# Kernel optimization log

Measured on AMD Instinct MI355X. Metric: run time of the kernel, lower is better.

Reference implementation:

```python
import jax, jax.numpy as jnp
import numpy as np


def apply_rotary_emb(x, freqs_cis):
    # x: [B, N, H, Dh], freqs_cis: [N, Dh//2, 2]
    B, N, H, Dh = x.shape
    x2 = x.reshape(B, N, H, Dh // 2, 2)
    f = freqs_cis[None, :, None]  # [1, N, 1, Dh//2, 2]
    real = x2[..., 0] * f[..., 0] - x2[..., 1] * f[..., 1]
    imag = x2[..., 1] * f[..., 0] + x2[..., 0] * f[..., 1]
    out = jnp.stack([real, imag], axis=-1)
    return out.reshape(B, N, H, Dh).astype(x.dtype)


def setup_inputs() -> dict:
    key = jax.random.key(0)
    k1, k2, k3, k4 = jax.random.split(key, 4)
    B, N, dim, n_head = 2, 2048, 2048, 16
    head_dim = dim // n_head
    x = jax.random.normal(k1, (B, N, dim), dtype=jnp.float32)
    # realistic rotary freqs (cos/sin), though random also works for correctness
    pos = jnp.arange(N, dtype=jnp.float32)[:, None]
    inv_freq = 1.0 / (10000.0 ** (jnp.arange(0, head_dim, 2, dtype=jnp.float32) / head_dim))
    ang = pos * inv_freq[None, :]  # [N, Dh//2]
    freqs_cis = jnp.stack([jnp.cos(ang), jnp.sin(ang)], axis=-1)  # [N, Dh//2, 2]
    wqkv = jax.random.normal(k2, (dim, 3 * dim), dtype=jnp.float32) * (dim ** -0.5)
    wo = jax.random.normal(k3, (dim, dim), dtype=jnp.float32) * (dim ** -0.5)
    return {"x": x, "freqs_cis": freqs_cis, "wqkv": wqkv, "wo": wo}


def reference(x, freqs_cis, wqkv, wo):
    B, N, dim = x.shape
    n_head = 16
    head_dim = dim // n_head
    qkv = x @ wqkv  # [B, N, 3*dim]
    q, k, v = jnp.split(qkv, 3, axis=-1)
    q = q.reshape(B, N, n_head, head_dim)
    k = k.reshape(B, N, n_head, head_dim)
    v = v.reshape(B, N, n_head, head_dim)
    q = apply_rotary_emb(q, freqs_cis)
    k = apply_rotary_emb(k, freqs_cis)
    scale = 1.0 / jnp.sqrt(jnp.asarray(head_dim, dtype=q.dtype))
    scores = jnp.einsum('bqhd,bkhd->bhqk', q, k) * scale
    attn = jax.nn.softmax(scores, axis=-1)
    out = jnp.einsum('bhqk,bkhd->bqhd', attn, v).reshape(B, N, dim)
    return out @ wo
```

## Files before the change

kernel.cpp:

```cpp
#include <hip/hip_runtime.h>
#include <hip/hip_bf16.h>
#include <stdint.h>

typedef __attribute__((ext_vector_type(8))) short bf16x8;
typedef __attribute__((ext_vector_type(4))) float f32x4;
typedef __attribute__((ext_vector_type(4))) unsigned short u16x4;
typedef __attribute__((ext_vector_type(8))) unsigned short u16x8;

#define DEV __device__ __forceinline__

DEV unsigned short f2bf(float f) {
  union { __hip_bfloat16 h; unsigned short u; } cv;
  cv.h = __float2bfloat16(f);
  return cv.u;
}

DEV void gload_lds16(const void* g, void* l) {
  __builtin_amdgcn_global_load_lds(
      (__attribute__((address_space(1))) void*)(uintptr_t)g,
      (__attribute__((address_space(3))) void*)(uint32_t)(uintptr_t)l,
      16, 0, 0);
}

__global__ __launch_bounds__(256) void k_convert(const float* __restrict__ in,
                                                 unsigned short* __restrict__ out,
                                                 int n8) {
  int i = blockIdx.x * 256 + threadIdx.x;
  if (i >= n8) return;
  const float4* p = (const float4*)in + (size_t)i * 2;
  float4 a = p[0], b = p[1];
  u16x8 o;
  o[0] = f2bf(a.x); o[1] = f2bf(a.y); o[2] = f2bf(a.z); o[3] = f2bf(a.w);
  o[4] = f2bf(b.x); o[5] = f2bf(b.y); o[6] = f2bf(b.z); o[7] = f2bf(b.w);
  *((u16x8*)out + (size_t)i) = o;
}

__global__ __launch_bounds__(256) void k_transpose_bf16(const float* __restrict__ in,
                                                        unsigned short* __restrict__ out,
                                                        int R, int C) {
  __shared__ float tile[32][33];
  const int t = threadIdx.x;
  const int c0 = blockIdx.x * 32, r0 = blockIdx.y * 32;
  {
    int r = t >> 3, c4 = (t & 7) * 4;
    float4 v = *(const float4*)&in[(size_t)(r0 + r) * C + c0 + c4];
    tile[r][c4] = v.x; tile[r][c4 + 1] = v.y; tile[r][c4 + 2] = v.z; tile[r][c4 + 3] = v.w;
  }
  __syncthreads();
  int c = t >> 3, r4 = (t & 7) * 4;
  u16x4 o;
  o[0] = f2bf(tile[r4 + 0][c]); o[1] = f2bf(tile[r4 + 1][c]);
  o[2] = f2bf(tile[r4 + 2][c]); o[3] = f2bf(tile[r4 + 3][c]);
  *(u16x4*)&out[(size_t)(c0 + c) * R + r0 + r4] = o;
}

__global__ __launch_bounds__(512, 2) void k_gemm_qkv(
    const unsigned short* __restrict__ A,
    const unsigned short* __restrict__ Bt,
    unsigned short* __restrict__ qb,
    unsigned short* __restrict__ kb,
    unsigned short* __restrict__ vt,
    const float* __restrict__ freqs) {
  constexpr int Kdim = 2048;
  __shared__ unsigned short As[2][16384];
  __shared__ unsigned short Bs[2][12288];
  const int t = threadIdx.x;
  const int lane = t & 63, wid = t >> 6;
  const int l15 = lane & 15, l4 = (lane >> 4) & 3;
  const int wm = wid >> 2, wn = wid & 3;
  const int bid = blockIdx.x;
  const int wg = (bid & 7) * 64 + (bid >> 3);
  const int by = wg & 15, bx = wg >> 4;
  const int m0 = by * 256, n0 = bx * 192;

  f32x4 acc[8][3];
#pragma unroll
  for (int i = 0; i < 8; i++)
#pragma unroll
    for (int j = 0; j < 3; j++) acc[i][j] = (f32x4)0.f;

  auto stageUA = [&](unsigned short* dstUnit, const unsigned short* src, int khalf) {
#pragma unroll
    for (int cb = 0; cb < 2; cb++) {
      int slotu = cb * 512 + wid * 64;
      int slot = slotu + lane;
      int row = slot >> 2, s = slot & 3;
      int c = s ^ ((row >> 1) & 3);
      gload_lds16(src + (size_t)row * Kdim + khalf * 32 + c * 8,
                  dstUnit + slotu * 8);
    }
  };
  auto stageUB = [&](unsigned short* dstUnit, const unsigned short* src, int khalf) {
    {
      int slotu = wid * 64;
      int slot = slotu + lane;
      int row = slot >> 2, s = slot & 3;
      int c = s ^ ((row >> 1) & 3);
      gload_lds16(src + (size_t)row * Kdim + khalf * 32 + c * 8,
                  dstUnit + slotu * 8);
    }
    {
      int slotu = 512 + (wid & 3) * 64;
      int slot = slotu + lane;
      int row = slot >> 2, s = slot & 3;
      int c = s ^ ((row >> 1) & 3);
      gload_lds16(src + (size_t)row * Kdim + khalf * 32 + c * 8,
                  dstUnit + slotu * 8);
    }
  };

  auto rdA2 = [&](int buf, int kk, int mh, bf16x8 (&f)[4]) {
    const unsigned short* base = &As[buf][kk * 8192];
#pragma unroll
    for (int mi = 0; mi < 4; mi++) {
      int row = wm * 128 + mh * 64 + mi * 16 + l15;
      int s = l4 ^ ((row >> 1) & 3);
      f[mi] = *(const bf16x8*)&base[row * 32 + s * 8];
    }
  };
  auto rdB2 = [&](int buf, int kk, bf16x8 (&f)[3]) {
    const unsigned short* base = &Bs[buf][kk * 6144];
#pragma unroll
    for (int ni = 0; ni < 3; ni++) {
      int row = wn * 48 + ni * 16 + l15;
      int s = l4 ^ ((row >> 1) & 3);
      f[ni] = *(const bf16x8*)&base[row * 32 + s * 8];
    }
  };
  auto mmaP = [&](bf16x8 (&a4)[4], bf16x8 (&b3)[3], int mib) {
    __builtin_amdgcn_s_setprio(1);
#pragma unroll
    for (int mi = 0; mi < 4; mi++)
#pragma unroll
      for (int ni = 0; ni < 3; ni++)
        acc[mib + mi][ni] = __builtin_amdgcn_mfma_f32_16x16x32_bf16(
            a4[mi], b3[ni], acc[mib + mi][ni], 0, 0, 0);
    __builtin_amdgcn_s_setprio(0);
  };

  const unsigned short* Abase = A + (size_t)m0 * Kdim;
  const unsigned short* Bbase = Bt + (size_t)n0 * Kdim;

  stageUA(&As[0][0], Abase, 0);
  stageUB(&Bs[0][0], Bbase, 0);
  stageUA(&As[0][8192], Abase, 1);
  stageUB(&Bs[0][6144], Bbase, 1);
  stageUA(&As[1][0], Abase + 64, 0);
  stageUB(&Bs[1][0], Bbase + 64, 0);
  asm volatile("s_waitcnt vmcnt(8)" ::: "memory");
  __builtin_amdgcn_s_barrier();

  bf16x8 a4[4], b3[3];
  for (int j = 0; j < 32; j++) {
    const int buf = j & 1;

    rdA2(buf, 0, 0, a4);
    rdB2(buf, 0, b3);
    if (j + 1 < 32) {
      stageUA(&As[buf ^ 1][8192], Abase + (j + 1) * 64, 1);
      stageUB(&Bs[buf ^ 1][6144], Bbase + (j + 1) * 64, 1);
    }
    __builtin_amdgcn_s_barrier();
    mmaP(a4, b3, 0);
    __builtin_amdgcn_s_barrier();

    rdA2(buf, 0, 1, a4);
    __builtin_amdgcn_s_barrier();
    mmaP(a4, b3, 4);
    if (j < 31) asm volatile("s_waitcnt vmcnt(8) lgkmcnt(0)" ::: "memory");
    else        asm volatile("s_waitcnt vmcnt(0) lgkmcnt(0)" ::: "memory");
    __builtin_amdgcn_s_barrier();

    rdA2(buf, 1, 0, a4);
    rdB2(buf, 1, b3);
    if (j + 2 < 32) {
      stageUA(&As[buf][0], Abase + (j + 2) * 64, 0);
      stageUB(&Bs[buf][0], Bbase + (j + 2) * 64, 0);
    }
    __builtin_amdgcn_s_barrier();
    mmaP(a4, b3, 0);
    __builtin_amdgcn_s_barrier();

    rdA2(buf, 1, 1, a4);
    __builtin_amdgcn_s_barrier();
    mmaP(a4, b3, 4);
    if (j < 30)       asm volatile("s_waitcnt vmcnt(8) lgkmcnt(0)" ::: "memory");
    else if (j == 30) asm volatile("s_waitcnt vmcnt(4) lgkmcnt(0)" ::: "memory");
    else              asm volatile("s_waitcnt lgkmcnt(0)" ::: "memory");
    __builtin_amdgcn_s_barrier();
  }

#pragma unroll
  for (int mi = 0; mi < 8; mi++) {
    int rowb = m0 + wm * 128 + mi * 16 + l4 * 4;
    int b = rowb >> 11;
    int tok0 = rowb & 2047;
#pragma unroll
    for (int ni = 0; ni < 3; ni++) {
      int col = n0 + wn * 48 + ni * 16 + l15;
      int sec = col >> 11;
      int h = (col >> 7) & 15;
      int dh = col & 127;
      if (sec == 2) {
        u16x4 o;
#pragma unroll
        for (int r = 0; r < 4; r++) o[r] = f2bf(acc[mi][ni][r]);
        *(u16x4*)&vt[((size_t)(b * 16 + h) * 128 + dh) * 2048 + tok0] = o;
      } else {
        unsigned short* dst = (sec == 0) ? qb : kb;
        int dh2 = dh >> 1;
        int odd = dh & 1;
#pragma unroll
        for (int r = 0; r < 4; r++) {
          float v = acc[mi][ni][r];
          float p = __shfl_xor(v, 1, 64);
          float2 cs = *(const float2*)&freqs[((size_t)(tok0 + r) * 64 + dh2) * 2];
          float o = odd ? (v * cs.x + p * cs.y) : (v * cs.x - p * cs.y);
          dst[((size_t)(b * 16 + h) * 2048 + tok0 + r) * 128 + dh] = f2bf(o);
        }
      }
    }
  }
}

__global__ __launch_bounds__(256) void k_gemm_out(
    const unsigned short* __restrict__ A,
    const unsigned short* __restrict__ Bt,
    int Kdim, int Nn,
    float* __restrict__ Cout) {
  __shared__ unsigned short As[128 * 64];
  __shared__ unsigned short Bs[128 * 64];
  const int t = threadIdx.x;
  const int lane = t & 63, wid = t >> 6;
  const int l15 = lane & 15, l4 = lane >> 4;
  const int m0 = blockIdx.y * 128, n0 = blockIdx.x * 128;
  const int wr = (wid >> 1) * 64, wc = (wid & 1) * 64;

  f32x4 acc[4][4];
#pragma unroll
  for (int i = 0; i < 4; i++)
#pragma unroll
    for (int j = 0; j < 4; j++) acc[i][j] = (f32x4)0.f;

  for (int k0 = 0; k0 < Kdim; k0 += 64) {
    __syncthreads();
#pragma unroll
    for (int j = 0; j < 4; j++) {
      int slotbase = j * 256 + wid * 64;
      int slot = slotbase + lane;
      int row = slot >> 3, cc = slot & 7;
      int cg = cc ^ (row & 7);
      gload_lds16(A + (size_t)(m0 + row) * Kdim + k0 + cg * 8, &As[slotbase * 8]);
      gload_lds16(Bt + (size_t)(n0 + row) * Kdim + k0 + cg * 8, &Bs[slotbase * 8]);
    }
    __syncthreads();
#pragma unroll
    for (int kk = 0; kk < 2; kk++) {
      bf16x8 af[4], bfr[4];
#pragma unroll
      for (int mi = 0; mi < 4; mi++) {
        int row = wr + mi * 16 + l15;
        int c = (kk * 4 + l4) ^ (row & 7);
        af[mi] = *(const bf16x8*)&As[row * 64 + c * 8];
      }
#pragma unroll
      for (int ni = 0; ni < 4; ni++) {
        int row = wc + ni * 16 + l15;
        int c = (kk * 4 + l4) ^ (row & 7);
        bfr[ni] = *(const bf16x8*)&Bs[row * 64 + c * 8];
      }
#pragma unroll
      for (int mi = 0; mi < 4; mi++)
#pragma unroll
        for (int ni = 0; ni < 4; ni++)
          acc[mi][ni] = __builtin_amdgcn_mfma_f32_16x16x32_bf16(af[mi], bfr[ni],
                                                                acc[mi][ni], 0, 0, 0);
    }
  }

#pragma unroll
  for (int mi = 0; mi < 4; mi++) {
    int rowb = m0 + wr + mi * 16 + l4 * 4;
#pragma unroll
    for (int ni = 0; ni < 4; ni++) {
      int col = n0 + wc + ni * 16 + l15;
#pragma unroll
      for (int r = 0; r < 4; r++)
        Cout[(size_t)(rowb + r) * Nn + col] = acc[mi][ni][r];
    }
  }
}

__global__ __launch_bounds__(256, 2) void k_attn(
    const unsigned short* __restrict__ qb,
    const unsigned short* __restrict__ kb,
    const unsigned short* __restrict__ vt,
    unsigned short* __restrict__ ao) {
  __shared__ unsigned short Ks[2][64 * 128];
  __shared__ unsigned short Vs[2][64 * 128];
  __shared__ unsigned short Ps[4][32 * 64];
  const int t = threadIdx.x;
  const int lane = t & 63, wid = t >> 6;
  const int l15 = lane & 15, l4 = lane >> 4;
  const int qt0 = blockIdx.x * 128;
  const int bh = blockIdx.y;
  const unsigned short* qbase = qb + (size_t)bh * 2048 * 128;
  const unsigned short* kbase = kb + (size_t)bh * 2048 * 128;
  const unsigned short* vbase = vt + (size_t)bh * 128 * 2048;

  bf16x8 qf[2][4];
#pragma unroll
  for (int mi = 0; mi < 2; mi++) {
    int qrow = qt0 + wid * 32 + mi * 16 + l15;
#pragma unroll
    for (int dk = 0; dk < 4; dk++)
      qf[mi][dk] = *(const bf16x8*)&qbase[(size_t)qrow * 128 + dk * 32 + l4 * 8];
  }

  f32x4 O[2][8];
#pragma unroll
  for (int mi = 0; mi < 2; mi++)
#pragma unroll
    for (int df = 0; df < 8; df++) O[mi][df] = (f32x4)0.f;
  float lsum[2][4];
#pragma unroll
  for (int mi = 0; mi < 2; mi++)
#pragma unroll
    for (int r = 0; r < 4; r++) lsum[mi][r] = 0.f;

  const float scale = 0.08838834764831845f;

  auto STAGE = [&](int kv0, int buf) {
#pragma unroll
    for (int j = 0; j < 4; j++) {
      int slotbase = j * 256 + wid * 64;
      int slot = slotbase + lane;
      int rowk = slot >> 4, ck = slot & 15;
      gload_lds16(&kbase[(size_t)(kv0 + rowk) * 128 + (ck ^ (rowk & 7)) * 8],
                  &Ks[buf][slotbase * 8]);
      int rowv = slot >> 3, cv = slot & 7;
      gload_lds16(&vbase[(size_t)rowv * 2048 + kv0 + (cv ^ (rowv & 7)) * 8],
                  &Vs[buf][slotbase * 8]);
    }
  };

  STAGE(0, 0);
  __syncthreads();

  for (int ti = 0; ti < 32; ti++) {
    const int cur = ti & 1;
    if (ti < 31) STAGE((ti + 1) * 64, cur ^ 1);

    f32x4 s[2][4];
#pragma unroll
    for (int mi = 0; mi < 2; mi++)
#pragma unroll
      for (int ni = 0; ni < 4; ni++) s[mi][ni] = (f32x4)0.f;
#pragma unroll
    for (int dk = 0; dk < 4; dk++) {
      bf16x8 kf[4];
#pragma unroll
      for (int ni = 0; ni < 4; ni++) {
        int row = ni * 16 + l15;
        int c = (dk * 4 + l4) ^ (row & 7);
        kf[ni] = *(const bf16x8*)&Ks[cur][row * 128 + c * 8];
      }
#pragma unroll
      for (int mi = 0; mi < 2; mi++)
#pragma unroll
        for (int ni = 0; ni < 4; ni++)
          s[mi][ni] = __builtin_amdgcn_mfma_f32_16x16x32_bf16(qf[mi][dk], kf[ni],
                                                              s[mi][ni], 0, 0, 0);
    }

    unsigned short* pbase = &Ps[wid][0];
#pragma unroll
    for (int mi = 0; mi < 2; mi++)
#pragma unroll
      for (int ni = 0; ni < 4; ni++) {
        int col = ni * 16 + l15;
#pragma unroll
        for (int r = 0; r < 4; r++) {
          float p = __expf(s[mi][ni][r] * scale);
          lsum[mi][r] += p;
          int rowp = mi * 16 + l4 * 4 + r;
          pbase[rowp * 64 + (((col >> 3) ^ (rowp & 7)) << 3) + (col & 7)] = f2bf(p);
        }
      }

    bf16x8 pf[2][2];
#pragma unroll
    for (int mi = 0; mi < 2; mi++)
#pragma unroll
      for (int kk = 0; kk < 2; kk++) {
        int row = mi * 16 + l15;
        int c = (kk * 4 + l4) ^ (row & 7);
        pf[mi][kk] = *(const bf16x8*)&pbase[row * 64 + c * 8];
      }

#pragma unroll
    for (int df = 0; df < 8; df++) {
      bf16x8 vf[2];
#pragma unroll
      for (int kk = 0; kk < 2; kk++) {
        int row = df * 16 + l15;
        int c = (kk * 4 + l4) ^ (row & 7);
        vf[kk] = *(const bf16x8*)&Vs[cur][row * 64 + c * 8];
      }
#pragma unroll
      for (int mi = 0; mi < 2; mi++)
#pragma unroll
        for (int kk = 0; kk < 2; kk++)
          O[mi][df] = __builtin_amdgcn_mfma_f32_16x16x32_bf16(pf[mi][kk], vf[kk],
                                                              O[mi][df], 0, 0, 0);
    }

    __syncthreads();
  }

  float inv[2][4];
#pragma unroll
  for (int mi = 0; mi < 2; mi++)
#pragma unroll
    for (int r = 0; r < 4; r++) {
      float v = lsum[mi][r];
      v += __shfl_xor(v, 1, 64);
      v += __shfl_xor(v, 2, 64);
      v += __shfl_xor(v, 4, 64);
      v += __shfl_xor(v, 8, 64);
      inv[mi][r] = 1.0f / v;
    }

  const int b = bh >> 4, h = bh & 15;
#pragma unroll
  for (int mi = 0; mi < 2; mi++)
#pragma unroll
    for (int df = 0; df < 8; df++)
#pragma unroll
      for (int r = 0; r < 4; r++) {
        int tok = qt0 + wid * 32 + mi * 16 + l4 * 4 + r;
        ao[((size_t)(b * 2048 + tok)) * 2048 + h * 128 + df * 16 + l15] =
            f2bf(O[mi][df][r] * inv[mi][r]);
      }
}

extern "C" void kernel_launch(void* const* d_in, const int* in_sizes, int n_in,
                              void* d_out, int out_size, void* d_ws, size_t ws_size,
                              hipStream_t stream) {
  const float* x     = (const float*)d_in[0];
  const float* freqs = (const float*)d_in[1];
  const float* wqkv  = (const float*)d_in[2];
  const float* wo    = (const float*)d_in[3];
  float* out = (float*)d_out;

  char* ws = (char*)d_ws;
  unsigned short* xb    = (unsigned short*)(ws + 0);
  unsigned short* wqkvT = (unsigned short*)(ws + 16777216);
  unsigned short* woT   = (unsigned short*)(ws + 41943040);
  unsigned short* qb    = (unsigned short*)(ws + 50331648);
  unsigned short* kb    = (unsigned short*)(ws + 67108864);
  unsigned short* vt    = (unsigned short*)(ws + 83886080);
  unsigned short* ao    = (unsigned short*)(ws + 100663296);

  k_convert<<<dim3(4096), dim3(256), 0, stream>>>(x, xb, 1048576);
  k_transpose_bf16<<<dim3(192, 64), dim3(256), 0, stream>>>(wqkv, wqkvT, 2048, 6144);
  k_transpose_bf16<<<dim3(64, 64), dim3(256), 0, stream>>>(wo, woT, 2048, 2048);

  k_gemm_qkv<<<dim3(512), dim3(512), 0, stream>>>(xb, wqkvT, qb, kb, vt, freqs);

  k_attn<<<dim3(16, 32), dim3(256), 0, stream>>>(qb, kb, vt, ao);

  k_gemm_out<<<dim3(16, 32), dim3(256), 0, stream>>>(ao, woT, 2048, 2048, out);
}
```

Baseline: 270.3 us.

## Enlarge attention tiles to 256 query rows and 128-key blocks with 8 waves

The attention kernel now runs 512-thread blocks, each covering 256 query rows, and stages 128 keys/values per iteration instead of 64. This halves the number of K/V tile loads from global memory per query row and halves the number of block-wide barriers. The P scratch buffer is shrunk to 16 rows per wave and processed in mi/half-tile chunks, so LDS use stays around 144KB with one block per CU. The cost is less scheduling slack: each CU holds only one large block and there are fewer blocks in the grid.

After: 279.0 us. 1.03x slower.

```diff
diff --git a/kernel.cpp b/kernel.cpp
--- a/kernel.cpp
+++ b/kernel.cpp
@@ -291,18 +291,18 @@
   }
 }
 
-__global__ __launch_bounds__(256, 2) void k_attn(
+__global__ __launch_bounds__(512, 1) void k_attn(
     const unsigned short* __restrict__ qb,
     const unsigned short* __restrict__ kb,
     const unsigned short* __restrict__ vt,
     unsigned short* __restrict__ ao) {
-  __shared__ unsigned short Ks[2][64 * 128];
-  __shared__ unsigned short Vs[2][64 * 128];
-  __shared__ unsigned short Ps[4][32 * 64];
+  __shared__ unsigned short Ks[2][128 * 128];
+  __shared__ unsigned short Vs[2][128 * 128];
+  __shared__ unsigned short Ps[8][16 * 64];
   const int t = threadIdx.x;
   const int lane = t & 63, wid = t >> 6;
   const int l15 = lane & 15, l4 = lane >> 4;
-  const int qt0 = blockIdx.x * 128;
+  const int qt0 = blockIdx.x * 256;
   const int bh = blockIdx.y;
   const unsigned short* qbase = qb + (size_t)bh * 2048 * 128;
   const unsigned short* kbase = kb + (size_t)bh * 2048 * 128;
@@ -333,12 +333,12 @@
   auto STAGE = [&](int kv0, int buf) {
 #pragma unroll
     for (int j = 0; j < 4; j++) {
-      int slotbase = j * 256 + wid * 64;
+      int slotbase = j * 512 + wid * 64;
       int slot = slotbase + lane;
       int rowk = slot >> 4, ck = slot & 15;
       gload_lds16(&kbase[(size_t)(kv0 + rowk) * 128 + (ck ^ (rowk & 7)) * 8],
                   &Ks[buf][slotbase * 8]);
-      int rowv = slot >> 3, cv = slot & 7;
+      int rowv = slot >> 4, cv = slot & 15;
       gload_lds16(&vbase[(size_t)rowv * 2048 + kv0 + (cv ^ (rowv & 7)) * 8],
                   &Vs[buf][slotbase * 8]);
     }
@@ -347,72 +347,65 @@
   STAGE(0, 0);
   __syncthreads();
 
-  for (int ti = 0; ti < 32; ti++) {
+  for (int ti = 0; ti < 16; ti++) {
     const int cur = ti & 1;
-    if (ti < 31) STAGE((ti + 1) * 64, cur ^ 1);
-
-    f32x4 s[2][4];
+    if (ti < 15) STAGE((ti + 1) * 128, cur ^ 1);
+
+    f32x4 s[2][8];
 #pragma unroll
     for (int mi = 0; mi < 2; mi++)
 #pragma unroll
-      for (int ni = 0; ni < 4; ni++) s[mi][ni] = (f32x4)0.f;
+      for (int ni = 0; ni < 8; ni++) s[mi][ni] = (f32x4)0.f;
 #pragma unroll
     for (int dk = 0; dk < 4; dk++) {
-      bf16x8 kf[4];
-#pragma unroll
-      for (int ni = 0; ni < 4; ni++) {
+#pragma unroll
+      for (int ni = 0; ni < 8; ni++) {
         int row = ni * 16 + l15;
         int c = (dk * 4 + l4) ^ (row & 7);
-        kf[ni] = *(const bf16x8*)&Ks[cur][row * 128 + c * 8];
-      }
-#pragma unroll
-      for (int mi = 0; mi < 2; mi++)
-#pragma unroll
-        for (int ni = 0; ni < 4; ni++)
-          s[mi][ni] = __builtin_amdgcn_mfma_f32_16x16x32_bf16(qf[mi][dk], kf[ni],
+        bf16x8 kf = *(const bf16x8*)&Ks[cur][row * 128 + c * 8];
+#pragma unroll
+        for (int mi = 0; mi < 2; mi++)
+          s[mi][ni] = __builtin_amdgcn_mfma_f32_16x16x32_bf16(qf[mi][dk], kf,
                                                               s[mi][ni], 0, 0, 0);
+      }
     }
 
     unsigned short* pbase = &Ps[wid][0];
 #pragma unroll
-    for (int mi = 0; mi < 2; mi++)
-#pragma unroll
-      for (int ni = 0; ni < 4; ni++) {
-        int col = ni * 16 + l15;
-#pragma unroll
-        for (int r = 0; r < 4; r++) {
-          float p = __expf(s[mi][ni][r] * scale);
-          lsum[mi][r] += p;
-          int rowp = mi * 16 + l4 * 4 + r;
-          pbase[rowp * 64 + (((col >> 3) ^ (rowp & 7)) << 3) + (col & 7)] = f2bf(p);
+    for (int mi = 0; mi < 2; mi++) {
+#pragma unroll
+      for (int hf = 0; hf < 2; hf++) {
+#pragma unroll
+        for (int nl = 0; nl < 4; nl++) {
+          int ni = hf * 4 + nl;
+          int ch = nl * 16 + l15;
+#pragma unroll
+          for (int r = 0; r < 4; r++) {
+            float p = __expf(s[mi][ni][r] * scale);
+            lsum[mi][r] += p;
+            int rowp = l4 * 4 + r;
+            pbase[rowp * 64 + (((ch >> 3) ^ (rowp & 7)) << 3) + (ch & 7)] = f2bf(p);
+          }
         }
-      }
-
-    bf16x8 pf[2][2];
-#pragma unroll
-    for (int mi = 0; mi < 2; mi++)
-#pragma unroll
-      for (int kk = 0; kk < 2; kk++) {
-        int row = mi * 16 + l15;
-        int c = (kk * 4 + l4) ^ (row & 7);
-        pf[mi][kk] = *(const bf16x8*)&pbase[row * 64 + c * 8];
-      }
-
-#pragma unroll
-    for (int df = 0; df < 8; df++) {
-      bf16x8 vf[2];
-#pragma unroll
-      for (int kk = 0; kk < 2; kk++) {
-        int row = df * 16 + l15;
-        int c = (kk * 4 + l4) ^ (row & 7);
-        vf[kk] = *(const bf16x8*)&Vs[cur][row * 64 + c * 8];
-      }
-#pragma unroll
-      for (int mi = 0; mi < 2; mi++)
-#pragma unroll
-        for (int kk = 0; kk < 2; kk++)
-          O[mi][df] = __builtin_amdgcn_mfma_f32_16x16x32_bf16(pf[mi][kk], vf[kk],
-                                                              O[mi][df], 0, 0, 0);
+        bf16x8 pf[2];
+#pragma unroll
+        for (int kl = 0; kl < 2; kl++) {
+          int c = (kl * 4 + l4) ^ (l15 & 7);
+          pf[kl] = *(const bf16x8*)&pbase[l15 * 64 + c * 8];
+        }
+#pragma unroll
+        for (int df = 0; df < 8; df++) {
+#pragma unroll
+          for (int kl = 0; kl < 2; kl++) {
+            int kk = hf * 2 + kl;
+            int row = df * 16 + l15;
+            int c = (kk * 4 + l4) ^ (row & 7);
+            bf16x8 vf = *(const bf16x8*)&Vs[cur][row * 128 + c * 8];
+            O[mi][df] = __builtin_amdgcn_mfma_f32_16x16x32_bf16(pf[kl], vf,
+                                                                O[mi][df], 0, 0, 0);
+          }
+        }
+      }
     }
 
     __syncthreads();
@@ -468,7 +461,7 @@
 
   k_gemm_qkv<<<dim3(512), dim3(512), 0, stream>>>(xb, wqkvT, qb, kb, vt, freqs);
 
-  k_attn<<<dim3(16, 32), dim3(256), 0, stream>>>(qb, kb, vt, ao);
+  k_attn<<<dim3(8, 32), dim3(512), 0, stream>>>(qb, kb, vt, ao);
 
   k_gemm_out<<<dim3(16, 32), dim3(256), 0, stream>>>(ao, woT, 2048, 2048, out);
 }
```

## Shrink QKV GEMM tile to 128x192 with 4 waves per block

Applied to the files above, without the earlier changes.

The QKV projection GEMM moves from 256x192 tiles with 8 waves to 128x192 tiles with 4 waves, launching 1024 blocks instead of 512. Each wave now computes a 64x96 sub-tile in one MFMA pass per k-half instead of two, which drops several barriers per iteration. The intent is to fill the GPU better and cut barrier overhead, in exchange for less operand reuse per block and more global traffic for the B tiles. The vmcnt wait counts are adjusted for the new number of loads.

After: 280.1 us. 3.6% more time.

```diff
diff --git a/kernel.cpp b/kernel.cpp
--- a/kernel.cpp
+++ b/kernel.cpp
@@ -54,7 +54,7 @@
   *(u16x4*)&out[(size_t)(c0 + c) * R + r0 + r4] = o;
 }
 
-__global__ __launch_bounds__(512, 2) void k_gemm_qkv(
+__global__ __launch_bounds__(256, 2) void k_gemm_qkv(
     const unsigned short* __restrict__ A,
     const unsigned short* __restrict__ Bt,
     unsigned short* __restrict__ qb,
@@ -62,27 +62,27 @@
     unsigned short* __restrict__ vt,
     const float* __restrict__ freqs) {
   constexpr int Kdim = 2048;
-  __shared__ unsigned short As[2][16384];
+  __shared__ unsigned short As[2][8192];
   __shared__ unsigned short Bs[2][12288];
   const int t = threadIdx.x;
   const int lane = t & 63, wid = t >> 6;
   const int l15 = lane & 15, l4 = (lane >> 4) & 3;
-  const int wm = wid >> 2, wn = wid & 3;
+  const int wm = wid >> 1, wn = wid & 1;
   const int bid = blockIdx.x;
-  const int wg = (bid & 7) * 64 + (bid >> 3);
-  const int by = wg & 15, bx = wg >> 4;
-  const int m0 = by * 256, n0 = bx * 192;
-
-  f32x4 acc[8][3];
-#pragma unroll
-  for (int i = 0; i < 8; i++)
-#pragma unroll
-    for (int j = 0; j < 3; j++) acc[i][j] = (f32x4)0.f;
+  const int wg = (bid & 7) * 128 + (bid >> 3);
+  const int by = wg & 31, bx = wg >> 5;
+  const int m0 = by * 128, n0 = bx * 192;
+
+  f32x4 acc[4][6];
+#pragma unroll
+  for (int i = 0; i < 4; i++)
+#pragma unroll
+    for (int j = 0; j < 6; j++) acc[i][j] = (f32x4)0.f;
 
   auto stageUA = [&](unsigned short* dstUnit, const unsigned short* src, int khalf) {
 #pragma unroll
     for (int cb = 0; cb < 2; cb++) {
-      int slotu = cb * 512 + wid * 64;
+      int slotu = cb * 256 + wid * 64;
       int slot = slotu + lane;
       int row = slot >> 2, s = slot & 3;
       int c = s ^ ((row >> 1) & 3);
@@ -91,50 +91,43 @@
     }
   };
   auto stageUB = [&](unsigned short* dstUnit, const unsigned short* src, int khalf) {
-    {
-      int slotu = wid * 64;
+#pragma unroll
+    for (int cb = 0; cb < 3; cb++) {
+      int slotu = cb * 256 + wid * 64;
       int slot = slotu + lane;
       int row = slot >> 2, s = slot & 3;
       int c = s ^ ((row >> 1) & 3);
       gload_lds16(src + (size_t)row * Kdim + khalf * 32 + c * 8,
                   dstUnit + slotu * 8);
     }
-    {
-      int slotu = 512 + (wid & 3) * 64;
-      int slot = slotu + lane;
-      int row = slot >> 2, s = slot & 3;
-      int c = s ^ ((row >> 1) & 3);
-      gload_lds16(src + (size_t)row * Kdim + khalf * 32 + c * 8,
-                  dstUnit + slotu * 8);
-    }
-  };
-
-  auto rdA2 = [&](int buf, int kk, int mh, bf16x8 (&f)[4]) {
-    const unsigned short* base = &As[buf][kk * 8192];
+  };
+
+  auto rdA2 = [&](int buf, int kk, bf16x8 (&f)[4]) {
+    const unsigned short* base = &As[buf][kk * 4096];
 #pragma unroll
     for (int mi = 0; mi < 4; mi++) {
-      int row = wm * 128 + mh * 64 + mi * 16 + l15;
+      int row = wm * 64 + mi * 16 + l15;
       int s = l4 ^ ((row >> 1) & 3);
       f[mi] = *(const bf16x8*)&base[row * 32 + s * 8];
     }
   };
-  auto rdB2 = [&](int buf, int kk, bf16x8 (&f)[3]) {
+  auto rdB2 = [&](int buf, int kk, bf16x8 (&f)[6]) {
     const unsigned short* base = &Bs[buf][kk * 6144];
 #pragma unroll
-    for (int ni = 0; ni < 3; ni++) {
-      int row = wn * 48 + ni * 16 + l15;
+    for (int ni = 0; ni < 6; ni++) {
+      int row = wn * 96 + ni * 16 + l15;
       int s = l4 ^ ((row >> 1) & 3);
       f[ni] = *(const bf16x8*)&base[row * 32 + s * 8];
     }
   };
-  auto mmaP = [&](bf16x8 (&a4)[4], bf16x8 (&b3)[3], int mib) {
+  auto mmaP = [&](bf16x8 (&a4)[4], bf16x8 (&b6)[6]) {
     __builtin_amdgcn_s_setprio(1);
 #pragma unroll
     for (int mi = 0; mi < 4; mi++)
 #pragma unroll
-      for (int ni = 0; ni < 3; ni++)
-        acc[mib + mi][ni] = __builtin_amdgcn_mfma_f32_16x16x32_bf16(
-            a4[mi], b3[ni], acc[mib + mi][ni], 0, 0, 0);
+      for (int ni = 0; ni < 6; ni++)
+        acc[mi][ni] = __builtin_amdgcn_mfma_f32_16x16x32_bf16(
+            a4[mi], b6[ni], acc[mi][ni], 0, 0, 0);
     __builtin_amdgcn_s_setprio(0);
   };
 
@@ -143,61 +136,50 @@
 
   stageUA(&As[0][0], Abase, 0);
   stageUB(&Bs[0][0], Bbase, 0);
-  stageUA(&As[0][8192], Abase, 1);
+  stageUA(&As[0][4096], Abase, 1);
   stageUB(&Bs[0][6144], Bbase, 1);
   stageUA(&As[1][0], Abase + 64, 0);
   stageUB(&Bs[1][0], Bbase + 64, 0);
-  asm volatile("s_waitcnt vmcnt(8)" ::: "memory");
+  asm volatile("s_waitcnt vmcnt(10)" ::: "memory");
   __builtin_amdgcn_s_barrier();
 
-  bf16x8 a4[4], b3[3];
+  bf16x8 a4[4], b6[6];
   for (int j = 0; j < 32; j++) {
     const int buf = j & 1;
 
-    rdA2(buf, 0, 0, a4);
-    rdB2(buf, 0, b3);
+    rdA2(buf, 0, a4);
+    rdB2(buf, 0, b6);
     if (j + 1 < 32) {
-      stageUA(&As[buf ^ 1][8192], Abase + (j + 1) * 64, 1);
+      stageUA(&As[buf ^ 1][4096], Abase + (j + 1) * 64, 1);
       stageUB(&Bs[buf ^ 1][6144], Bbase + (j + 1) * 64, 1);
     }
     __builtin_amdgcn_s_barrier();
-    mmaP(a4, b3, 0);
+    mmaP(a4, b6);
+    if (j < 31) asm volatile("s_waitcnt vmcnt(10)" ::: "memory");
+    else        asm volatile("s_waitcnt vmcnt(0)" ::: "memory");
     __builtin_amdgcn_s_barrier();
 
-    rdA2(buf, 0, 1, a4);
-    __builtin_amdgcn_s_barrier();
-    mmaP(a4, b3, 4);
-    if (j < 31) asm volatile("s_waitcnt vmcnt(8) lgkmcnt(0)" ::: "memory");
-    else        asm volatile("s_waitcnt vmcnt(0) lgkmcnt(0)" ::: "memory");
-    __builtin_amdgcn_s_barrier();
-
-    rdA2(buf, 1, 0, a4);
-    rdB2(buf, 1, b3);
+    rdA2(buf, 1, a4);
+    rdB2(buf, 1, b6);
     if (j + 2 < 32) {
       stageUA(&As[buf][0], Abase + (j + 2) * 64, 0);
       stageUB(&Bs[buf][0], Bbase + (j + 2) * 64, 0);
     }
     __builtin_amdgcn_s_barrier();
-    mmaP(a4, b3, 0);
+    mmaP(a4, b6);
+    if (j < 30)       asm volatile("s_waitcnt vmcnt(10)" ::: "memory");
+    else if (j == 30) asm volatile("s_waitcnt vmcnt(5)" ::: "memory");
     __builtin_amdgcn_s_barrier();
-
-    rdA2(buf, 1, 1, a4);
-    __builtin_amdgcn_s_barrier();
-    mmaP(a4, b3, 4);
-    if (j < 30)       asm volatile("s_waitcnt vmcnt(8) lgkmcnt(0)" ::: "memory");
-    else if (j == 30) asm volatile("s_waitcnt vmcnt(4) lgkmcnt(0)" ::: "memory");
-    else              asm volatile("s_waitcnt lgkmcnt(0)" ::: "memory");
-    __builtin_amdgcn_s_barrier();
-  }
-
-#pragma unroll
-  for (int mi = 0; mi < 8; mi++) {
-    int rowb = m0 + wm * 128 + mi * 16 + l4 * 4;
+  }
+
+#pragma unroll
+  for (int mi = 0; mi < 4; mi++) {
+    int rowb = m0 + wm * 64 + mi * 16 + l4 * 4;
     int b = rowb >> 11;
     int tok0 = rowb & 2047;
 #pragma unroll
-    for (int ni = 0; ni < 3; ni++) {
-      int col = n0 + wn * 48 + ni * 16 + l15;
+    for (int ni = 0; ni < 6; ni++) {
+      int col = n0 + wn * 96 + ni * 16 + l15;
       int sec = col >> 11;
       int h = (col >> 7) & 15;
       int dh = col & 127;
@@ -466,7 +448,7 @@
   k_transpose_bf16<<<dim3(192, 64), dim3(256), 0, stream>>>(wqkv, wqkvT, 2048, 6144);
   k_transpose_bf16<<<dim3(64, 64), dim3(256), 0, stream>>>(wo, woT, 2048, 2048);
 
-  k_gemm_qkv<<<dim3(512), dim3(512), 0, stream>>>(xb, wqkvT, qb, kb, vt, freqs);
+  k_gemm_qkv<<<dim3(1024), dim3(256), 0, stream>>>(xb, wqkvT, qb, kb, vt, freqs);
 
   k_attn<<<dim3(16, 32), dim3(256), 0, stream>>>(qb, kb, vt, ao);
 
```

## Pipeline output GEMM with double-buffered LDS and XCD-aware block remap

Applied to the files above, without the earlier changes.

Rewrites the output projection GEMM to split each K tile into two 32-wide halves and prefetch them into double-buffered shared memory with fine-grained vmcnt waits, so global loads overlap MFMA work. It also remaps the linear block index so neighbouring tiles land on the same XCD for L2 reuse, raises MFMA priority, and hardcodes the dimensions. The manual waitcnt/barrier scheme is fragile and doubles LDS use, which may limit occupancy.

Measured after the change: 273.5 us. No clear change (+1.2%).

```diff
diff --git a/kernel.cpp b/kernel.cpp
--- a/kernel.cpp
+++ b/kernel.cpp
@@ -223,18 +223,21 @@
   }
 }
 
-__global__ __launch_bounds__(256) void k_gemm_out(
+__global__ __launch_bounds__(256, 2) void k_gemm_out(
     const unsigned short* __restrict__ A,
     const unsigned short* __restrict__ Bt,
-    int Kdim, int Nn,
     float* __restrict__ Cout) {
-  __shared__ unsigned short As[128 * 64];
-  __shared__ unsigned short Bs[128 * 64];
+  constexpr int Kdim = 2048, Nn = 2048;
+  __shared__ unsigned short As[2][8192];
+  __shared__ unsigned short Bs[2][8192];
   const int t = threadIdx.x;
   const int lane = t & 63, wid = t >> 6;
-  const int l15 = lane & 15, l4 = lane >> 4;
-  const int m0 = blockIdx.y * 128, n0 = blockIdx.x * 128;
-  const int wr = (wid >> 1) * 64, wc = (wid & 1) * 64;
+  const int l15 = lane & 15, l4 = (lane >> 4) & 3;
+  const int wm = wid >> 1, wn = wid & 1;
+  const int bid = blockIdx.x;
+  const int wg = (bid & 7) * 64 + (bid >> 3);
+  const int by = wg & 31, bx = wg >> 5;
+  const int m0 = by * 128, n0 = bx * 128;
 
   f32x4 acc[4][4];
 #pragma unroll
@@ -242,48 +245,83 @@
 #pragma unroll
     for (int j = 0; j < 4; j++) acc[i][j] = (f32x4)0.f;
 
-  for (int k0 = 0; k0 < Kdim; k0 += 64) {
-    __syncthreads();
-#pragma unroll
-    for (int j = 0; j < 4; j++) {
-      int slotbase = j * 256 + wid * 64;
-      int slot = slotbase + lane;
-      int row = slot >> 3, cc = slot & 7;
-      int cg = cc ^ (row & 7);
-      gload_lds16(A + (size_t)(m0 + row) * Kdim + k0 + cg * 8, &As[slotbase * 8]);
-      gload_lds16(Bt + (size_t)(n0 + row) * Kdim + k0 + cg * 8, &Bs[slotbase * 8]);
-    }
-    __syncthreads();
-#pragma unroll
-    for (int kk = 0; kk < 2; kk++) {
-      bf16x8 af[4], bfr[4];
-#pragma unroll
-      for (int mi = 0; mi < 4; mi++) {
-        int row = wr + mi * 16 + l15;
-        int c = (kk * 4 + l4) ^ (row & 7);
-        af[mi] = *(const bf16x8*)&As[row * 64 + c * 8];
-      }
-#pragma unroll
-      for (int ni = 0; ni < 4; ni++) {
-        int row = wc + ni * 16 + l15;
-        int c = (kk * 4 + l4) ^ (row & 7);
-        bfr[ni] = *(const bf16x8*)&Bs[row * 64 + c * 8];
-      }
-#pragma unroll
-      for (int mi = 0; mi < 4; mi++)
-#pragma unroll
-        for (int ni = 0; ni < 4; ni++)
-          acc[mi][ni] = __builtin_amdgcn_mfma_f32_16x16x32_bf16(af[mi], bfr[ni],
-                                                                acc[mi][ni], 0, 0, 0);
-    }
+  auto stageU = [&](unsigned short* dstUnit, const unsigned short* src, int khalf) {
+#pragma unroll
+    for (int cb = 0; cb < 2; cb++) {
+      int slotu = cb * 256 + wid * 64;
+      int slot = slotu + lane;
+      int row = slot >> 2, s = slot & 3;
+      int c = s ^ ((row >> 1) & 3);
+      gload_lds16(src + (size_t)row * Kdim + khalf * 32 + c * 8,
+                  dstUnit + slotu * 8);
+    }
+  };
+  auto rd4 = [&](const unsigned short* base, int w, bf16x8 (&f)[4]) {
+#pragma unroll
+    for (int i = 0; i < 4; i++) {
+      int row = w * 64 + i * 16 + l15;
+      int s = l4 ^ ((row >> 1) & 3);
+      f[i] = *(const bf16x8*)&base[row * 32 + s * 8];
+    }
+  };
+  auto mma16 = [&](bf16x8 (&a4)[4], bf16x8 (&b4)[4]) {
+    __builtin_amdgcn_s_setprio(1);
+#pragma unroll
+    for (int mi = 0; mi < 4; mi++)
+#pragma unroll
+      for (int ni = 0; ni < 4; ni++)
+        acc[mi][ni] = __builtin_amdgcn_mfma_f32_16x16x32_bf16(
+            a4[mi], b4[ni], acc[mi][ni], 0, 0, 0);
+    __builtin_amdgcn_s_setprio(0);
+  };
+
+  const unsigned short* Abase = A + (size_t)m0 * Kdim;
+  const unsigned short* Bbase = Bt + (size_t)n0 * Kdim;
+
+  stageU(&As[0][0], Abase, 0);
+  stageU(&Bs[0][0], Bbase, 0);
+  stageU(&As[0][4096], Abase, 1);
+  stageU(&Bs[0][4096], Bbase, 1);
+  stageU(&As[1][0], Abase + 64, 0);
+  stageU(&Bs[1][0], Bbase + 64, 0);
+  asm volatile("s_waitcnt vmcnt(8)" ::: "memory");
+  __builtin_amdgcn_s_barrier();
+
+  bf16x8 a4[4], b4[4];
+  for (int j = 0; j < 32; j++) {
+    const int buf = j & 1;
+
+    rd4(&As[buf][0], wm, a4);
+    rd4(&Bs[buf][0], wn, b4);
+    if (j + 1 < 32) {
+      stageU(&As[buf ^ 1][4096], Abase + (j + 1) * 64, 1);
+      stageU(&Bs[buf ^ 1][4096], Bbase + (j + 1) * 64, 1);
+    }
+    __builtin_amdgcn_s_barrier();
+    mma16(a4, b4);
+    if (j < 31) asm volatile("s_waitcnt vmcnt(8)" ::: "memory");
+    else        asm volatile("s_waitcnt vmcnt(0)" ::: "memory");
+    __builtin_amdgcn_s_barrier();
+
+    rd4(&As[buf][4096], wm, a4);
+    rd4(&Bs[buf][4096], wn, b4);
+    if (j + 2 < 32) {
+      stageU(&As[buf][0], Abase + (j + 2) * 64, 0);
+      stageU(&Bs[buf][0], Bbase + (j + 2) * 64, 0);
+    }
+    __builtin_amdgcn_s_barrier();
+    mma16(a4, b4);
+    if (j < 30)       asm volatile("s_waitcnt vmcnt(8)" ::: "memory");
+    else if (j == 30) asm volatile("s_waitcnt vmcnt(4)" ::: "memory");
+    __builtin_amdgcn_s_barrier();
   }
 
 #pragma unroll
   for (int mi = 0; mi < 4; mi++) {
-    int rowb = m0 + wr + mi * 16 + l4 * 4;
+    int rowb = m0 + wm * 64 + mi * 16 + l4 * 4;
 #pragma unroll
     for (int ni = 0; ni < 4; ni++) {
-      int col = n0 + wc + ni * 16 + l15;
+      int col = n0 + wn * 64 + ni * 16 + l15;
 #pragma unroll
       for (int r = 0; r < 4; r++)
         Cout[(size_t)(rowb + r) * Nn + col] = acc[mi][ni][r];
@@ -470,5 +508,5 @@
 
   k_attn<<<dim3(16, 32), dim3(256), 0, stream>>>(qb, kb, vt, ao);
 
-  k_gemm_out<<<dim3(16, 32), dim3(256), 0, stream>>>(ao, woT, 2048, 2048, out);
-}
+  k_gemm_out<<<dim3(512), dim3(256), 0, stream>>>(ao, woT, out);
+}
```
